# Performance work log

Hardware: AMD Instinct MI355X
Metric: run time of the kernel (lower is better)

## Reference

```python
import jax, jax.numpy as jnp
import numpy as np

B, S, D, H, DFF = 2, 2048, 1024, 16, 4096
DK = D // H
EPS = 1e-6


def setup_inputs() -> dict:
    key = jax.random.key(0)
    ks = jax.random.split(key, 16)
    sd = 0.02
    inp = {
        "x": jax.random.normal(ks[0], (B, S, D), jnp.float32),
        "mask": jnp.zeros((1, 1, S, S), jnp.float32),
        "wq": jax.random.normal(ks[1], (D, D), jnp.float32) * sd,
        "bq": jnp.zeros((D,), jnp.float32),
        "wk": jax.random.normal(ks[2], (D, D), jnp.float32) * sd,
        "bk": jnp.zeros((D,), jnp.float32),
        "wv": jax.random.normal(ks[3], (D, D), jnp.float32) * sd,
        "bv": jnp.zeros((D,), jnp.float32),
        "wo": jax.random.normal(ks[4], (D, D), jnp.float32) * sd,
        "bo": jnp.zeros((D,), jnp.float32),
        "w1": jax.random.normal(ks[5], (DFF, D), jnp.float32) * sd,
        "b1": jnp.zeros((DFF,), jnp.float32),
        "w2": jax.random.normal(ks[6], (D, DFF), jnp.float32) * sd,
        "b2": jnp.zeros((D,), jnp.float32),
        "alpha": jnp.ones((1,), jnp.float32),
        "gamma": jnp.zeros((1,), jnp.float32),
    }
    return inp


def _layer_norm(x, alpha, gamma):
    mean = jnp.mean(x, axis=-1, keepdims=True)
    var = jnp.mean((x - mean) ** 2, axis=-1, keepdims=True)
    return alpha * (x - mean) / jnp.sqrt(var + EPS) + gamma


def reference(x, mask, wq, bq, wk, bk, wv, bv, wo, bo, w1, b1, w2, b2, alpha, gamma):
    # --- multi-head attention (hand-rolled, full NxN scores) ---
    q = (x @ wq.T + bq).reshape(B, S, H, DK).transpose(0, 2, 1, 3)  # [B,H,S,DK]
    k = (x @ wk.T + bk).reshape(B, S, H, DK).transpose(0, 2, 1, 3)
    v = (x @ wv.T + bv).reshape(B, S, H, DK).transpose(0, 2, 1, 3)
    scores = jnp.einsum('bhqd,bhkd->bhqk', q, k) / np.sqrt(DK)  # [B,H,S,S]
    scores = scores + mask
    attn = jax.nn.softmax(scores, axis=-1)
    ctx = jnp.einsum('bhqk,bhkd->bhqd', attn, v)  # [B,H,S,DK]
    ctx = ctx.transpose(0, 2, 1, 3).reshape(B, S, D)
    attn_out = ctx @ wo.T + bo
    # residual + LayerNorm (dropout is identity in eval)
    out1 = _layer_norm(x + attn_out, alpha, gamma)
    # --- position-wise feed-forward ---
    ffn = jax.nn.relu(out1 @ w1.T + b1) @ w2.T + b2
    out2 = _layer_norm(out1 + ffn, alpha, gamma)
    return out2
```

## Files before the change

### kernel.cpp

```cpp
#include <hip/hip_runtime.h>


typedef float  f32x4   __attribute__((ext_vector_type(4)));
typedef float  f32x16  __attribute__((ext_vector_type(16)));
typedef __bf16 bf16x8  __attribute__((ext_vector_type(8)));
typedef __bf16 bf16x4  __attribute__((ext_vector_type(4)));

#define DEVI static __device__ __forceinline__

DEVI f32x4 mfma16(bf16x8 a, bf16x8 b, f32x4 c) {
    return __builtin_amdgcn_mfma_f32_16x16x32_bf16(a, b, c, 0, 0, 0);
}
DEVI f32x16 mfma32(bf16x8 a, bf16x8 b, f32x16 c) {
    return __builtin_amdgcn_mfma_f32_32x32x16_bf16(a, b, c, 0, 0, 0);
}

DEVI void gll16(const void* g, void* l) {
    __builtin_amdgcn_global_load_lds(
        (__attribute__((address_space(1))) void*)g,
        (__attribute__((address_space(3))) void*)l, 16, 0, 0);
}

DEVI __bf16 f2bf(float f) { return (__bf16)f; }

DEVI unsigned cvtpk_bf16(float a, float b) {
    unsigned d;
    asm("v_cvt_pk_bf16_f32 %0, %1, %2" : "=v"(d) : "v"(a), "v"(b));
    return d;
}
DEVI void permswap(unsigned& a, unsigned& b) {
    asm("v_permlane32_swap_b32 %0, %1" : "+v"(a), "+v"(b));
}
DEVI void permswapf(float& a, float& b) {
    asm("v_permlane32_swap_b32 %0, %1" : "+v"(a), "+v"(b));
}

__global__ void init_flag_kernel(int* f) { *f = 0; }

__global__ void mask_scan_kernel(const float* __restrict__ m, int* __restrict__ flag) {
    size_t i = (size_t)blockIdx.x * 256 + threadIdx.x;
    const float4* p = (const float4*)m;
    float4 a = p[i * 2], b = p[i * 2 + 1];
    bool nz = a.x != 0.f || a.y != 0.f || a.z != 0.f || a.w != 0.f ||
              b.x != 0.f || b.y != 0.f || b.z != 0.f || b.w != 0.f;
    if (__ballot(nz)) { if ((threadIdx.x & 63) == 0) atomicOr(flag, 1); }
}

__global__ void cast_bf16_kernel(const float* __restrict__ in, __bf16* __restrict__ out, int n8) {
    int i = blockIdx.x * 256 + threadIdx.x;
    if (i >= n8) return;
    const float4* p = (const float4*)in + (size_t)i * 2;
    float4 a = p[0], b = p[1];
    bf16x8 o = { (__bf16)a.x, (__bf16)a.y, (__bf16)a.z, (__bf16)a.w,
                 (__bf16)b.x, (__bf16)b.y, (__bf16)b.z, (__bf16)b.w };
    *(bf16x8*)(out + (size_t)i * 8) = o;
}

__global__ __launch_bounds__(256) void add_ln_kernel(
    const float* __restrict__ X, const float* __restrict__ Y,
    const float* __restrict__ alphap, const float* __restrict__ gammap,
    float* __restrict__ outF, __bf16* __restrict__ outB) {
    const int tid = threadIdx.x, lane = tid & 63, wid = tid >> 6;
    const size_t base = (size_t)blockIdx.x * 1024 + tid * 4;
    float4 xv = *(const float4*)&X[base];
    float4 yv = *(const float4*)&Y[base];
    float vx = xv.x + yv.x, vy = xv.y + yv.y, vz = xv.z + yv.z, vw = xv.w + yv.w;
    float s = vx + vy + vz + vw;
    #pragma unroll
    for (int o = 32; o; o >>= 1) s += __shfl_xor(s, o);
    __shared__ float red[4];
    if (lane == 0) red[wid] = s;
    __syncthreads();
    float mean = (red[0] + red[1] + red[2] + red[3]) * (1.0f / 1024.0f);
    float dx = vx - mean, dy = vy - mean, dz = vz - mean, dw = vw - mean;
    float s2 = dx * dx + dy * dy + dz * dz + dw * dw;
    #pragma unroll
    for (int o = 32; o; o >>= 1) s2 += __shfl_xor(s2, o);
    __syncthreads();
    if (lane == 0) red[wid] = s2;
    __syncthreads();
    float var = (red[0] + red[1] + red[2] + red[3]) * (1.0f / 1024.0f);
    float rstd = rsqrtf(var + 1e-6f);
    float a = alphap[0], g = gammap[0];
    float4 o4 = { a * dx * rstd + g, a * dy * rstd + g, a * dz * rstd + g, a * dw * rstd + g };
    *(float4*)&outF[base] = o4;
    if (outB) {
        bf16x4 ob = { f2bf(o4.x), f2bf(o4.y), f2bf(o4.z), f2bf(o4.w) };
        *(bf16x4*)&outB[base] = ob;
    }
}

template <int N, int K, int BN, int MODE>
__global__ __launch_bounds__(256, 2) void gemm_bt_kernel(
    const __bf16* __restrict__ A, const __bf16* __restrict__ W,
    const float* __restrict__ bias, void* __restrict__ outp) {
    constexpr int WN = BN / 2;
    constexpr int NI = WN / 16;
    __shared__ __bf16 lsA[128 * 64];
    __shared__ __bf16 lsB[BN * 64];
    const int tid = threadIdx.x, wid = tid >> 6, lane = tid & 63;
    const int wr = wid >> 1, wc = wid & 1, l15 = lane & 15, hi = lane >> 4;
    const int m0 = blockIdx.y * 128, n0 = blockIdx.x * BN;
    f32x4 acc[4][NI] = {};
    for (int kt = 0; kt < K / 64; ++kt) {
        #pragma unroll
        for (int i = 0; i < 4; ++i) {
            int row = wid * 32 + i * 8 + (lane >> 3);
            gll16(A + (size_t)(m0 + row) * K + kt * 64 + ((lane & 7) ^ (row & 7)) * 8,
                  &lsA[(wid * 32 + i * 8) * 64]);
        }
        #pragma unroll
        for (int i = 0; i < BN / 32; ++i) {
            int row = wid * (BN / 4) + i * 8 + (lane >> 3);
            gll16(W + (size_t)(n0 + row) * K + kt * 64 + ((lane & 7) ^ (row & 7)) * 8,
                  &lsB[(wid * (BN / 4) + i * 8) * 64]);
        }
        __syncthreads();
        #pragma unroll
        for (int s = 0; s < 2; ++s) {
            bf16x8 af[4], bfv[NI];
            #pragma unroll
            for (int mi = 0; mi < 4; ++mi) {
                int row = wr * 64 + mi * 16 + l15;
                af[mi] = *(const bf16x8*)&lsA[row * 64 + (((s * 4 + hi) ^ (row & 7)) * 8)];
            }
            #pragma unroll
            for (int ni = 0; ni < NI; ++ni) {
                int row = wc * WN + ni * 16 + l15;
                bfv[ni] = *(const bf16x8*)&lsB[row * 64 + (((s * 4 + hi) ^ (row & 7)) * 8)];
            }
            #pragma unroll
            for (int mi = 0; mi < 4; ++mi)
                #pragma unroll
                for (int ni = 0; ni < NI; ++ni)
                    acc[mi][ni] = mfma16(af[mi], bfv[ni], acc[mi][ni]);
        }
        __syncthreads();
    }
    #pragma unroll
    for (int ni = 0; ni < NI; ++ni) {
        int col = n0 + wc * WN + ni * 16 + l15;
        float bv = bias[col];
        #pragma unroll
        for (int mi = 0; mi < 4; ++mi) {
            int rowb = m0 + wr * 64 + mi * 16 + hi * 4;
            #pragma unroll
            for (int r = 0; r < 4; ++r) {
                float v = acc[mi][ni][r] + bv;
                if (MODE == 0) {
                    ((float*)outp)[(size_t)(rowb + r) * N + col] = v;
                } else {
                    v = fmaxf(v, 0.f);
                    ((__bf16*)outp)[(size_t)(rowb + r) * N + col] = f2bf(v);
                }
            }
        }
    }
}

__global__ __launch_bounds__(256, 2) void gemm_qkv_kernel(
    const __bf16* __restrict__ A,
    const __bf16* __restrict__ wq, const __bf16* __restrict__ wk, const __bf16* __restrict__ wv,
    const float* __restrict__ bq, const float* __restrict__ bk, const float* __restrict__ bv,
    __bf16* __restrict__ q, __bf16* __restrict__ k, __bf16* __restrict__ vt) {
    constexpr int K = 1024;
    const int z = blockIdx.z;
    const __bf16* W = (z == 0) ? wq : (z == 1) ? wk : wv;
    const float* bias = (z == 0) ? bq : (z == 1) ? bk : bv;
    __shared__ __bf16 lsA[128 * 64];
    __shared__ __bf16 lsB[128 * 64];
    const int tid = threadIdx.x, wid = tid >> 6, lane = tid & 63;
    const int wr = wid >> 1, wc = wid & 1, l15 = lane & 15, hi = lane >> 4;
    const int m0 = blockIdx.y * 128, n0 = blockIdx.x * 128;
    f32x4 acc[4][4] = {};
    for (int kt = 0; kt < K / 64; ++kt) {
        #pragma unroll
        for (int i = 0; i < 4; ++i) {
            int row = wid * 32 + i * 8 + (lane >> 3);
            gll16(A + (size_t)(m0 + row) * K + kt * 64 + ((lane & 7) ^ (row & 7)) * 8,
                  &lsA[(wid * 32 + i * 8) * 64]);
            gll16(W + (size_t)(n0 + row) * K + kt * 64 + ((lane & 7) ^ (row & 7)) * 8,
                  &lsB[(wid * 32 + i * 8) * 64]);
        }
        __syncthreads();
        #pragma unroll
        for (int s = 0; s < 2; ++s) {
            bf16x8 af[4], bfv[4];
            #pragma unroll
            for (int mi = 0; mi < 4; ++mi) {
                int row = wr * 64 + mi * 16 + l15;
                af[mi] = *(const bf16x8*)&lsA[row * 64 + (((s * 4 + hi) ^ (row & 7)) * 8)];
            }
            #pragma unroll
            for (int ni = 0; ni < 4; ++ni) {
                int row = wc * 64 + ni * 16 + l15;
                bfv[ni] = *(const bf16x8*)&lsB[row * 64 + (((s * 4 + hi) ^ (row & 7)) * 8)];
            }
            #pragma unroll
            for (int mi = 0; mi < 4; ++mi)
                #pragma unroll
                for (int ni = 0; ni < 4; ++ni)
                    acc[mi][ni] = mfma16(af[mi], bfv[ni], acc[mi][ni]);
        }
        __syncthreads();
    }
    const float scale = (z == 0) ? 0.125f * 1.4426950408889634f : 1.0f;
    #pragma unroll
    for (int ni = 0; ni < 4; ++ni) {
        int col = n0 + wc * 64 + ni * 16 + l15;
        int h = col >> 6, dk = col & 63;
        float bvv = bias[col];
        #pragma unroll
        for (int mi = 0; mi < 4; ++mi) {
            int rowb = m0 + wr * 64 + mi * 16 + hi * 4;
            int b_ = rowb >> 11, sb = rowb & 2047;
            if (z < 2) {
                __bf16* dst = (z == 0) ? q : k;
                #pragma unroll
                for (int r = 0; r < 4; ++r)
                    dst[((size_t)(b_ * 16 + h) * 2048 + sb + r) * 64 + dk] =
                        f2bf((acc[mi][ni][r] + bvv) * scale);
            } else {
                bf16x4 o = { f2bf(acc[mi][ni][0] + bvv), f2bf(acc[mi][ni][1] + bvv),
                             f2bf(acc[mi][ni][2] + bvv), f2bf(acc[mi][ni][3] + bvv) };
                *(bf16x4*)&vt[((size_t)(b_ * 16 + h) * 64 + dk) * 2048 + sb] = o;
            }
        }
    }
}

__global__ __launch_bounds__(256, 2) void flash_attn_kernel(
    const __bf16* __restrict__ Q, const __bf16* __restrict__ Kx,
    const __bf16* __restrict__ VT, const float* __restrict__ mask,
    const int* __restrict__ mflag, __bf16* __restrict__ ctx) {
    __shared__ __bf16 Kl[64 * 64];
    __shared__ __bf16 Vl[64 * 64];
    const int lane = threadIdx.x & 63, wid = threadIdx.x >> 6;
    const int l31 = lane & 31, h = lane >> 5;
    const int id = blockIdx.x;
    const int xcd = id & 7, rest = id >> 3;
    const int qt = rest & 15;
    const int bh = (rest >> 4) * 8 + xcd;
    const int q0 = qt * 128 + wid * 32;

    bf16x8 qf[4];
    const size_t qrow = (size_t)bh * 2048 + q0 + l31;
    #pragma unroll
    for (int st = 0; st < 4; ++st)
        qf[st] = *(const bf16x8*)&Q[qrow * 64 + st * 16 + h * 8];

    const __bf16* kbase = Kx + (size_t)bh * 2048 * 64;
    const __bf16* vbase = VT + (size_t)bh * 64 * 2048;

    f32x16 c0 = {}, c1 = {};
    float mrun = -1e30f, lrun = 0.f;
    const bool useMask = (*mflag != 0);

    const int r0 = wid * 16;
    const int rA = r0 + (lane >> 3);
    const int rB = r0 + 8 + (lane >> 3);
    const int cA = (lane & 7) ^ (rA & 7);
    const int cB = (lane & 7) ^ (rB & 7);

    for (int t = 0; t < 32; ++t) {
        gll16(kbase + (size_t)(t * 64 + rA) * 64 + cA * 8, &Kl[r0 * 64]);
        gll16(kbase + (size_t)(t * 64 + rB) * 64 + cB * 8, &Kl[(r0 + 8) * 64]);
        gll16(vbase + (size_t)rA * 2048 + t * 64 + cA * 8, &Vl[r0 * 64]);
        gll16(vbase + (size_t)rB * 2048 + t * 64 + cB * 8, &Vl[(r0 + 8) * 64]);
        __syncthreads();
        #pragma unroll
        for (int s = 0; s < 2; ++s) {
            const int krow = s * 32 + l31;
            f32x16 sc = {};
            #pragma unroll
            for (int st = 0; st < 4; ++st) {
                bf16x8 kf = *(const bf16x8*)&Kl[krow * 64 + (((st * 2 + h) ^ (krow & 7)) * 8)];
                sc = mfma32(kf, qf[st], sc);
            }
            if (useMask) {
                #pragma unroll
                for (int r = 0; r < 16; ++r) {
                    int kv = t * 64 + s * 32 + (r & 3) + 8 * (r >> 2) + 4 * h;
                    sc[r] += mask[(size_t)(q0 + l31) * 2048 + kv] * 1.4426950408889634f;
                }
            }
            float x8[8], x4[4];
            #pragma unroll
            for (int r = 0; r < 8; ++r) x8[r] = fmaxf(sc[2 * r], sc[2 * r + 1]);
            #pragma unroll
            for (int r = 0; r < 4; ++r) x4[r] = fmaxf(x8[2 * r], x8[2 * r + 1]);
            float tm = fmaxf(fmaxf(x4[0], x4[1]), fmaxf(x4[2], x4[3]));
            { float a = tm, b = tm; permswapf(a, b); tm = fmaxf(a, b); }
            if (!__all(tm <= mrun + 8.0f)) {
                float mn = fmaxf(mrun, tm);
                float fac = exp2f(mrun - mn);
                mrun = mn; lrun *= fac;
                #pragma unroll
                for (int r = 0; r < 16; ++r) { c0[r] *= fac; c1[r] *= fac; }
            }
            #pragma unroll
            for (int r = 0; r < 16; ++r) sc[r] = exp2f(sc[r] - mrun);
            float y8[8], y4[4];
            #pragma unroll
            for (int r = 0; r < 8; ++r) y8[r] = sc[2 * r] + sc[2 * r + 1];
            #pragma unroll
            for (int r = 0; r < 4; ++r) y4[r] = y8[2 * r] + y8[2 * r + 1];
            float ts = (y4[0] + y4[1]) + (y4[2] + y4[3]);
            { float a = ts, b = ts; permswapf(a, b); ts = a + b; }
            lrun += ts;
            unsigned w0 = cvtpk_bf16(sc[0], sc[1]),   w2 = cvtpk_bf16(sc[4], sc[5]);
            unsigned w1 = cvtpk_bf16(sc[2], sc[3]),   w3 = cvtpk_bf16(sc[6], sc[7]);
            permswap(w0, w2); permswap(w1, w3);
            unsigned w4 = cvtpk_bf16(sc[8], sc[9]),   w6 = cvtpk_bf16(sc[12], sc[13]);
            unsigned w5 = cvtpk_bf16(sc[10], sc[11]), w7 = cvtpk_bf16(sc[14], sc[15]);
            permswap(w4, w6); permswap(w5, w7);
            uint4 u0 = { w0, w1, w2, w3 }, u1 = { w4, w5, w6, w7 };
            bf16x8 pb0, pb1;
            __builtin_memcpy(&pb0, &u0, 16);
            __builtin_memcpy(&pb1, &u1, 16);
            const int vr0 = l31, vr1 = 32 + l31;
            bf16x8 v00 = *(const bf16x8*)&Vl[vr0 * 64 + (((s * 4 + 0 + h) ^ (vr0 & 7)) * 8)];
            bf16x8 v01 = *(const bf16x8*)&Vl[vr0 * 64 + (((s * 4 + 2 + h) ^ (vr0 & 7)) * 8)];
            bf16x8 v10 = *(const bf16x8*)&Vl[vr1 * 64 + (((s * 4 + 0 + h) ^ (vr1 & 7)) * 8)];
            bf16x8 v11 = *(const bf16x8*)&Vl[vr1 * 64 + (((s * 4 + 2 + h) ^ (vr1 & 7)) * 8)];
            c0 = mfma32(v00, pb0, c0);
            c0 = mfma32(v01, pb1, c0);
            c1 = mfma32(v10, pb0, c1);
            c1 = mfma32(v11, pb1, c1);
        }
        __syncthreads();
    }

    const float rinv = 1.0f / lrun;
    const int b_ = bh >> 4, h_ = bh & 15;
    const size_t obase = ((size_t)b_ * 2048 + q0 + l31) * 1024 + (size_t)h_ * 64;
    #pragma unroll
    for (int g = 0; g < 4; ++g) {
        bf16x4 o0 = { f2bf(c0[4 * g + 0] * rinv), f2bf(c0[4 * g + 1] * rinv),
                      f2bf(c0[4 * g + 2] * rinv), f2bf(c0[4 * g + 3] * rinv) };
        *(bf16x4*)&ctx[obase + g * 8 + h * 4] = o0;
        bf16x4 o1 = { f2bf(c1[4 * g + 0] * rinv), f2bf(c1[4 * g + 1] * rinv),
                      f2bf(c1[4 * g + 2] * rinv), f2bf(c1[4 * g + 3] * rinv) };
        *(bf16x4*)&ctx[obase + 32 + g * 8 + h * 4] = o1;
    }
}

extern "C" void kernel_launch(void* const* d_in, const int* in_sizes, int n_in,
                              void* d_out, int out_size, void* d_ws, size_t ws_size,
                              hipStream_t stream) {
    const float* x     = (const float*)d_in[0];
    const float* mask  = (const float*)d_in[1];
    const float* wq    = (const float*)d_in[2];
    const float* bq    = (const float*)d_in[3];
    const float* wk    = (const float*)d_in[4];
    const float* bk    = (const float*)d_in[5];
    const float* wv    = (const float*)d_in[6];
    const float* bv    = (const float*)d_in[7];
    const float* wo    = (const float*)d_in[8];
    const float* bo    = (const float*)d_in[9];
    const float* w1    = (const float*)d_in[10];
    const float* b1    = (const float*)d_in[11];
    const float* w2    = (const float*)d_in[12];
    const float* b2    = (const float*)d_in[13];
    const float* alpha = (const float*)d_in[14];
    const float* gamma = (const float*)d_in[15];

    char* ws = (char*)d_ws;
    const size_t MB = 1u << 20;
    __bf16* xb    = (__bf16*)(ws + 0 * MB);
    __bf16* qb    = (__bf16*)(ws + 8 * MB);
    __bf16* kb    = (__bf16*)(ws + 16 * MB);
    __bf16* vtb   = (__bf16*)(ws + 24 * MB);
    __bf16* ctxb  = (__bf16*)(ws + 32 * MB);
    __bf16* wqb   = (__bf16*)(ws + 40 * MB);
    __bf16* wkb   = (__bf16*)(ws + 42 * MB);
    __bf16* wvb   = (__bf16*)(ws + 44 * MB);
    __bf16* wob   = (__bf16*)(ws + 46 * MB);
    __bf16* w1b   = (__bf16*)(ws + 48 * MB);
    __bf16* w2b   = (__bf16*)(ws + 56 * MB);
    float*  attn  = (float*)(ws + 64 * MB);
    float*  out1  = (float*)(ws + 80 * MB);
    __bf16* out1b = (__bf16*)(ws + 96 * MB);
    __bf16* hid   = (__bf16*)(ws + 104 * MB);
    int*    mflag = (int*)(ws + 136 * MB);
    if (ws_size < 136 * MB + 64) return;

    init_flag_kernel<<<1, 1, 0, stream>>>(mflag);
    mask_scan_kernel<<<2048, 256, 0, stream>>>(mask, mflag);

    cast_bf16_kernel<<<2048, 256, 0, stream>>>(x, xb, 524288);
    cast_bf16_kernel<<<512, 256, 0, stream>>>(wq, wqb, 131072);
    cast_bf16_kernel<<<512, 256, 0, stream>>>(wk, wkb, 131072);
    cast_bf16_kernel<<<512, 256, 0, stream>>>(wv, wvb, 131072);
    cast_bf16_kernel<<<512, 256, 0, stream>>>(wo, wob, 131072);
    cast_bf16_kernel<<<2048, 256, 0, stream>>>(w1, w1b, 524288);
    cast_bf16_kernel<<<2048, 256, 0, stream>>>(w2, w2b, 524288);

    gemm_qkv_kernel<<<dim3(8, 32, 3), 256, 0, stream>>>(xb, wqb, wkb, wvb, bq, bk, bv,
                                                        qb, kb, vtb);
    flash_attn_kernel<<<dim3(512), 256, 0, stream>>>(qb, kb, vtb, mask, mflag, ctxb);
    gemm_bt_kernel<1024, 1024, 64, 0><<<dim3(16, 32), 256, 0, stream>>>(ctxb, wob, bo, attn);
    add_ln_kernel<<<4096, 256, 0, stream>>>(x, attn, alpha, gamma, out1, out1b);
    gemm_bt_kernel<4096, 1024, 128, 1><<<dim3(32, 32), 256, 0, stream>>>(out1b, w1b, b1, hid);
    gemm_bt_kernel<1024, 4096, 64, 0><<<dim3(16, 32), 256, 0, stream>>>(hid, w2b, b2, attn);
    add_ln_kernel<<<4096, 256, 0, stream>>>(out1, attn, alpha, gamma, (float*)d_out, nullptr);
}
```

Before: 280.6 us.

## Double-buffer K/V tiles in flash attention and raise MFMA wave priority

The flash attention kernel now keeps two LDS buffers for K and V and issues the async global-to-LDS loads for tile t+1 before computing on tile t, so memory latency overlaps with MFMA work instead of stalling at a barrier before each tile. It also wraps the MFMA sections in s_setprio to favour matrix issue. This doubles LDS use per block (32KB), which may affect occupancy, and the last iteration redundantly reloads the final tile. Since global_load_lds completion is tracked via vmcnt, the single barrier at the end of each iteration may not guarantee the prefetched data has landed before it is read.

```diff
diff --git a/kernel.cpp b/kernel.cpp
--- a/kernel.cpp
+++ b/kernel.cpp
@@ -233,8 +233,8 @@
     const __bf16* __restrict__ Q, const __bf16* __restrict__ Kx,
     const __bf16* __restrict__ VT, const float* __restrict__ mask,
     const int* __restrict__ mflag, __bf16* __restrict__ ctx) {
-    __shared__ __bf16 Kl[64 * 64];
-    __shared__ __bf16 Vl[64 * 64];
+    __shared__ __bf16 Kl[2][64 * 64];
+    __shared__ __bf16 Vl[2][64 * 64];
     const int lane = threadIdx.x & 63, wid = threadIdx.x >> 6;
     const int l31 = lane & 31, h = lane >> 5;
     const int id = blockIdx.x;
@@ -258,25 +258,35 @@
 
     const int r0 = wid * 16;
     const int rA = r0 + (lane >> 3);
-    const int rB = r0 + 8 + (lane >> 3);
+    const int rB = rA + 8;
     const int cA = (lane & 7) ^ (rA & 7);
     const int cB = (lane & 7) ^ (rB & 7);
 
+    auto stage = [&](int b, int t) {
+        gll16(kbase + (size_t)(t * 64 + rA) * 64 + cA * 8, &Kl[b][r0 * 64]);
+        gll16(kbase + (size_t)(t * 64 + rB) * 64 + cB * 8, &Kl[b][(r0 + 8) * 64]);
+        gll16(vbase + (size_t)rA * 2048 + t * 64 + cA * 8, &Vl[b][r0 * 64]);
+        gll16(vbase + (size_t)rB * 2048 + t * 64 + cB * 8, &Vl[b][(r0 + 8) * 64]);
+    };
+
+    stage(0, 0);
+    __syncthreads();
+    int cur = 0;
+
     for (int t = 0; t < 32; ++t) {
-        gll16(kbase + (size_t)(t * 64 + rA) * 64 + cA * 8, &Kl[r0 * 64]);
-        gll16(kbase + (size_t)(t * 64 + rB) * 64 + cB * 8, &Kl[(r0 + 8) * 64]);
-        gll16(vbase + (size_t)rA * 2048 + t * 64 + cA * 8, &Vl[r0 * 64]);
-        gll16(vbase + (size_t)rB * 2048 + t * 64 + cB * 8, &Vl[(r0 + 8) * 64]);
-        __syncthreads();
+        const int tn = (t + 1 < 32) ? t + 1 : t;
+        stage(cur ^ 1, tn);
         #pragma unroll
         for (int s = 0; s < 2; ++s) {
             const int krow = s * 32 + l31;
             f32x16 sc = {};
+            __builtin_amdgcn_s_setprio(1);
             #pragma unroll
             for (int st = 0; st < 4; ++st) {
-                bf16x8 kf = *(const bf16x8*)&Kl[krow * 64 + (((st * 2 + h) ^ (krow & 7)) * 8)];
+                bf16x8 kf = *(const bf16x8*)&Kl[cur][krow * 64 + (((st * 2 + h) ^ (krow & 7)) * 8)];
                 sc = mfma32(kf, qf[st], sc);
             }
+            __builtin_amdgcn_s_setprio(0);
             if (useMask) {
                 #pragma unroll
                 for (int r = 0; r < 16; ++r) {
@@ -319,16 +329,19 @@
             __builtin_memcpy(&pb0, &u0, 16);
             __builtin_memcpy(&pb1, &u1, 16);
             const int vr0 = l31, vr1 = 32 + l31;
-            bf16x8 v00 = *(const bf16x8*)&Vl[vr0 * 64 + (((s * 4 + 0 + h) ^ (vr0 & 7)) * 8)];
-            bf16x8 v01 = *(const bf16x8*)&Vl[vr0 * 64 + (((s * 4 + 2 + h) ^ (vr0 & 7)) * 8)];
-            bf16x8 v10 = *(const bf16x8*)&Vl[vr1 * 64 + (((s * 4 + 0 + h) ^ (vr1 & 7)) * 8)];
-            bf16x8 v11 = *(const bf16x8*)&Vl[vr1 * 64 + (((s * 4 + 2 + h) ^ (vr1 & 7)) * 8)];
+            bf16x8 v00 = *(const bf16x8*)&Vl[cur][vr0 * 64 + (((s * 4 + 0 + h) ^ (vr0 & 7)) * 8)];
+            bf16x8 v01 = *(const bf16x8*)&Vl[cur][vr0 * 64 + (((s * 4 + 2 + h) ^ (vr0 & 7)) * 8)];
+            bf16x8 v10 = *(const bf16x8*)&Vl[cur][vr1 * 64 + (((s * 4 + 0 + h) ^ (vr1 & 7)) * 8)];
+            bf16x8 v11 = *(const bf16x8*)&Vl[cur][vr1 * 64 + (((s * 4 + 2 + h) ^ (vr1 & 7)) * 8)];
+            __builtin_amdgcn_s_setprio(1);
             c0 = mfma32(v00, pb0, c0);
             c0 = mfma32(v01, pb1, c0);
             c1 = mfma32(v10, pb0, c1);
             c1 = mfma32(v11, pb1, c1);
+            __builtin_amdgcn_s_setprio(0);
         }
         __syncthreads();
+        cur ^= 1;
     }
 
     const float rinv = 1.0f / lrun;
```

After: 278.8 us. About the same (-0.7%).
